# Optimization experiments

Hardware: AMD Instinct MI355X
Metric: run time of the kernel (lower is better)

The kernel has to match this reference:

```python
import jax, jax.numpy as jnp
import numpy as np

T_THRESH = 1.0  # t_thresh init arg


def _step_fn(x):
    # Heaviside forward (gradient handled separately in bwd module)
    return (x > 0).astype(x.dtype)


def setup_inputs() -> dict:
    key = jax.random.key(0)
    k1, = jax.random.split(key, 1)
    x = jax.random.normal(k1, (64, 500, 1024), dtype=jnp.float32)
    w_input = jnp.asarray(1.0, dtype=jnp.float32)
    w_leak = jnp.asarray(0.1, dtype=jnp.float32)
    return {"x": x, "w_input": w_input, "w_leak": w_leak}


def reference(x, w_input, w_leak):
    # Leaky integrate-and-fire over time axis (axis=1).
    # Vm_t = relu(w_i * x_t + (1 - w_l) * Vm_{t-1} * step(t_thresh - Vm_{t-1}))
    # spike_t = step(Vm_t - t_thresh)
    def step(Vm, xt):  # Vm, xt: [B, C]
        forget = _step_fn(T_THRESH - Vm)  # reset if Vm crossed threshold
        Vm = jax.nn.relu(w_input * xt + (1.0 - w_leak) * Vm * forget)
        spike = _step_fn(Vm - T_THRESH)
        return Vm, spike

    Vm0 = jnp.zeros_like(x[:, 0])  # [B, C]
    xt = jnp.swapaxes(x, 0, 1)  # [T, B, C]
    _, spikes = jax.lax.scan(step, Vm0, xt)
    return jnp.swapaxes(spikes, 0, 1)  # [B, T, C]
```

## Files before the change

kernel.cpp:

```cpp
#include <hip/hip_runtime.h>


#define LIF_B 64
#define LIF_T 500
#define LIF_C 1024
#define LIF_U 20
#define LIF_NCH (LIF_T / LIF_U)

__global__ __launch_bounds__(256) void lif_kernel(
    const float* __restrict__ x,
    const float* __restrict__ w_input_p,
    const float* __restrict__ w_leak_p,
    float* __restrict__ out) {

  const int tid = blockIdx.x * blockDim.x + threadIdx.x;
  const int b = tid >> 10;
  const int c = tid & (LIF_C - 1);

  const float wi = w_input_p[0];
  const float kl = __fsub_rn(1.0f, w_leak_p[0]);

  const float* xp = x   + (size_t)b * LIF_T * LIF_C + c;
  float*       op = out + (size_t)b * LIF_T * LIF_C + c;

  float buf[2][LIF_U];

#pragma unroll
  for (int u = 0; u < LIF_U; ++u) {
    buf[0][u] = xp[(size_t)u * LIF_C];
  }

  float Vm = 0.0f;

  for (int k = 0; k < LIF_NCH; ++k) {
    const int cur = k & 1;

    if (k + 1 < LIF_NCH) {
      const float* xn = xp + (size_t)(k + 1) * LIF_U * LIF_C;
#pragma unroll
      for (int u = 0; u < LIF_U; ++u) {
        buf[cur ^ 1][u] = xn[(size_t)u * LIF_C];
      }
    }

    float* on = op + (size_t)k * LIF_U * LIF_C;
#pragma unroll
    for (int u = 0; u < LIF_U; ++u) {
      const float xt = buf[cur][u];
      const float acc = (Vm < 1.0f) ? __fmul_rn(kl, Vm) : 0.0f;
      const float v   = __fadd_rn(__fmul_rn(wi, xt), acc);
      Vm = fmaxf(v, 0.0f);
      on[(size_t)u * LIF_C] = (Vm > 1.0f) ? 1.0f : 0.0f;
    }
  }
}

extern "C" void kernel_launch(void* const* d_in, const int* in_sizes, int n_in,
                              void* d_out, int out_size, void* d_ws, size_t ws_size,
                              hipStream_t stream) {
  const float* x  = (const float*)d_in[0];
  const float* wi = (const float*)d_in[1];
  const float* wl = (const float*)d_in[2];
  float* out = (float*)d_out;

  const int n_threads = LIF_B * LIF_C;
  const int block = 256;
  const int grid = n_threads / block;
  lif_kernel<<<grid, block, 0, stream>>>(x, wi, wl, out);
}
```

Measured before the change: 243.9 us.

## Deepen register prefetch pipeline to four rotating chunk buffers

Replaces the two-buffer register prefetch with four rotating 25-step buffers, so up to three chunks of future inputs are in flight while one chunk is computed. With only 65536 threads and about four waves per CU, the scan is latency-bound, and more outstanding loads per thread should hide memory latency better. It also sets launch bounds to one block per SM minimum, letting the compiler spend many more VGPRs on the buffers. The risk is register pressure or spills, and the compiler reordering the loads despite the asm memory barriers.

New measurement: 234.4 us. -3.9%, faster.

```diff
diff --git a/kernel.cpp b/kernel.cpp
--- a/kernel.cpp
+++ b/kernel.cpp
@@ -4,10 +4,33 @@
 #define LIF_B 64
 #define LIF_T 500
 #define LIF_C 1024
-#define LIF_U 20
+#define LIF_U 25
 #define LIF_NCH (LIF_T / LIF_U)
 
-__global__ __launch_bounds__(256) void lif_kernel(
+#define PREFETCH(buf, kk)                                     \
+  do {                                                        \
+    const float* xn = xp + (size_t)(kk) * LIF_U * LIF_C;      \
+    _Pragma("unroll")                                         \
+    for (int u = 0; u < LIF_U; ++u) {                         \
+      buf[u] = xn[(size_t)u * LIF_C];                         \
+    }                                                         \
+    __asm__ volatile("" ::: "memory");                        \
+  } while (0)
+
+#define COMPUTE(buf, kk)                                      \
+  do {                                                        \
+    float* on = op + (size_t)(kk) * LIF_U * LIF_C;            \
+    _Pragma("unroll")                                         \
+    for (int u = 0; u < LIF_U; ++u) {                         \
+      const float xt = buf[u];                                \
+      const float acc = (Vm < 1.0f) ? __fmul_rn(kl, Vm) : 0.0f; \
+      const float v   = __fadd_rn(__fmul_rn(wi, xt), acc);    \
+      Vm = fmaxf(v, 0.0f);                                    \
+      on[(size_t)u * LIF_C] = (Vm > 1.0f) ? 1.0f : 0.0f;      \
+    }                                                         \
+  } while (0)
+
+__global__ __launch_bounds__(256, 1) void lif_kernel(
     const float* __restrict__ x,
     const float* __restrict__ w_input_p,
     const float* __restrict__ w_leak_p,
@@ -23,35 +46,25 @@
   const float* xp = x   + (size_t)b * LIF_T * LIF_C + c;
   float*       op = out + (size_t)b * LIF_T * LIF_C + c;
 
-  float buf[2][LIF_U];
-
-#pragma unroll
-  for (int u = 0; u < LIF_U; ++u) {
-    buf[0][u] = xp[(size_t)u * LIF_C];
-  }
-
+  float bufA[LIF_U];
+  float bufB[LIF_U];
+  float bufC[LIF_U];
+  float bufD[LIF_U];
   float Vm = 0.0f;
 
-  for (int k = 0; k < LIF_NCH; ++k) {
-    const int cur = k & 1;
+  PREFETCH(bufA, 0);
+  PREFETCH(bufB, 1);
+  PREFETCH(bufC, 2);
 
-    if (k + 1 < LIF_NCH) {
-      const float* xn = xp + (size_t)(k + 1) * LIF_U * LIF_C;
-#pragma unroll
-      for (int u = 0; u < LIF_U; ++u) {
-        buf[cur ^ 1][u] = xn[(size_t)u * LIF_C];
-      }
-    }
-
-    float* on = op + (size_t)k * LIF_U * LIF_C;
-#pragma unroll
-    for (int u = 0; u < LIF_U; ++u) {
-      const float xt = buf[cur][u];
-      const float acc = (Vm < 1.0f) ? __fmul_rn(kl, Vm) : 0.0f;
-      const float v   = __fadd_rn(__fmul_rn(wi, xt), acc);
-      Vm = fmaxf(v, 0.0f);
-      on[(size_t)u * LIF_C] = (Vm > 1.0f) ? 1.0f : 0.0f;
-    }
+  for (int k = 0; k < LIF_NCH; k += 4) {
+    PREFETCH(bufD, k + 3);
+    COMPUTE(bufA, k);
+    if (k + 4 < LIF_NCH) PREFETCH(bufA, k + 4);
+    COMPUTE(bufB, k + 1);
+    if (k + 5 < LIF_NCH) PREFETCH(bufB, k + 5);
+    COMPUTE(bufC, k + 2);
+    if (k + 6 < LIF_NCH) PREFETCH(bufC, k + 6);
+    COMPUTE(bufD, k + 3);
   }
 }
 
```

## Stage input chunks into LDS with async global_load_lds double buffering

Applied to the files above, without the earlier changes.

Replaces per-thread register double-buffered global loads with cooperative direct global-to-LDS 16-byte async loads (global_load_lds) into a double-buffered shared-memory tile of 25 timesteps by 256 channels. Each thread then reads its column from LDS during the sequential recurrence. The goal is to cut register pressure and issue fewer, wider load instructions while prefetching the next chunk. It adds a block barrier per chunk and relies on the async LDS load completing before the barrier, which the code does not wait on explicitly (no vmcnt wait), so correctness depends on the compiler inserting it.

New measurement: 231.6 us. 5.1% less time.

```diff
diff --git a/kernel.cpp b/kernel.cpp
--- a/kernel.cpp
+++ b/kernel.cpp
@@ -4,8 +4,12 @@
 #define LIF_B 64
 #define LIF_T 500
 #define LIF_C 1024
-#define LIF_U 20
-#define LIF_NCH (LIF_T / LIF_U)
+#define LIF_TC 25
+#define LIF_NCH (LIF_T / LIF_TC)
+#define LIF_BC 256
+
+#define GLOBAL_AS(p) ((__attribute__((address_space(1))) const void*)(uintptr_t)(p))
+#define LDS_AS(p)    ((__attribute__((address_space(3))) void*)(uintptr_t)(p))
 
 __global__ __launch_bounds__(256) void lif_kernel(
     const float* __restrict__ x,
@@ -13,44 +17,50 @@
     const float* __restrict__ w_leak_p,
     float* __restrict__ out) {
 
-  const int tid = blockIdx.x * blockDim.x + threadIdx.x;
-  const int b = tid >> 10;
-  const int c = tid & (LIF_C - 1);
+  __shared__ float lds[2][LIF_TC * LIF_BC];
+
+  const int b     = blockIdx.x >> 2;
+  const int cbase = (blockIdx.x & 3) << 8;
+  const int tidx  = threadIdx.x;
+  const int wave  = tidx >> 6;
+  const int lane  = tidx & 63;
 
   const float wi = w_input_p[0];
   const float kl = __fsub_rn(1.0f, w_leak_p[0]);
 
-  const float* xp = x   + (size_t)b * LIF_T * LIF_C + c;
-  float*       op = out + (size_t)b * LIF_T * LIF_C + c;
+  const float* xblk = x   + (size_t)b * LIF_T * LIF_C + cbase;
+  float*       oblk = out + (size_t)b * LIF_T * LIF_C + cbase;
 
-  float buf[2][LIF_U];
+  auto stage = [&](int k, int p) {
+    const float* src0 = xblk + (size_t)k * LIF_TC * LIF_C;
+#pragma unroll
+    for (int r0 = 0; r0 < LIF_TC; r0 += 4) {
+      const int r = r0 + wave;
+      if (r < LIF_TC) {
+        const float* g = src0 + (size_t)r * LIF_C + lane * 4;
+        float* l = &lds[p][r * LIF_BC];
+        __builtin_amdgcn_global_load_lds(GLOBAL_AS(g), LDS_AS(l), 16, 0, 0);
+      }
+    }
+  };
 
-#pragma unroll
-  for (int u = 0; u < LIF_U; ++u) {
-    buf[0][u] = xp[(size_t)u * LIF_C];
-  }
+  stage(0, 0);
 
   float Vm = 0.0f;
 
   for (int k = 0; k < LIF_NCH; ++k) {
-    const int cur = k & 1;
+    const int p = k & 1;
+    __syncthreads();
+    if (k + 1 < LIF_NCH) stage(k + 1, p ^ 1);
 
-    if (k + 1 < LIF_NCH) {
-      const float* xn = xp + (size_t)(k + 1) * LIF_U * LIF_C;
+    float* orow = oblk + (size_t)k * LIF_TC * LIF_C + tidx;
 #pragma unroll
-      for (int u = 0; u < LIF_U; ++u) {
-        buf[cur ^ 1][u] = xn[(size_t)u * LIF_C];
-      }
-    }
-
-    float* on = op + (size_t)k * LIF_U * LIF_C;
-#pragma unroll
-    for (int u = 0; u < LIF_U; ++u) {
-      const float xt = buf[cur][u];
+    for (int r = 0; r < LIF_TC; ++r) {
+      const float xt  = lds[p][r * LIF_BC + tidx];
       const float acc = (Vm < 1.0f) ? __fmul_rn(kl, Vm) : 0.0f;
       const float v   = __fadd_rn(__fmul_rn(wi, xt), acc);
       Vm = fmaxf(v, 0.0f);
-      on[(size_t)u * LIF_C] = (Vm > 1.0f) ? 1.0f : 0.0f;
+      orow[(size_t)r * LIF_C] = (Vm > 1.0f) ? 1.0f : 0.0f;
     }
   }
 }
@@ -63,8 +73,6 @@
   const float* wl = (const float*)d_in[2];
   float* out = (float*)d_out;
 
-  const int n_threads = LIF_B * LIF_C;
-  const int block = 256;
-  const int grid = n_threads / block;
-  lif_kernel<<<grid, block, 0, stream>>>(x, wi, wl, out);
+  const int grid = LIF_B * (LIF_C / LIF_BC);
+  lif_kernel<<<grid, 256, 0, stream>>>(x, wi, wl, out);
 }
```
